# Optimization experiments

Hardware: AMD Instinct MI355X
Metric: run time of the kernel (lower is better)

## Reference

```python
import jax, jax.numpy as jnp
import numpy as np

N_NODES = 50000
N_EDGES = 800000
DIM = 64
BN_EPS = 1e-5


def setup_inputs() -> dict:
    key = jax.random.key(0)
    ks = jax.random.split(key, 9)
    s = 1.0 / np.sqrt(DIM)
    feature = jax.random.normal(ks[0], (N_NODES, DIM), jnp.float32)
    edge_index = jax.random.randint(ks[1], (2, N_EDGES), 0, N_NODES)
    Wk = jax.random.normal(ks[2], (DIM, DIM), jnp.float32) * s
    Wq = jax.random.normal(ks[3], (DIM, DIM), jnp.float32) * s
    Wv = jax.random.normal(ks[4], (DIM, DIM), jnp.float32) * s
    bk = jax.random.normal(ks[5], (DIM,), jnp.float32) * 0.01
    bq = jax.random.normal(ks[6], (DIM,), jnp.float32) * 0.01
    bv = jax.random.normal(ks[7], (DIM,), jnp.float32) * 0.01
    bias = jax.random.normal(ks[8], (DIM,), jnp.float32) * 0.01
    gamma = jnp.ones((DIM,), jnp.float32)
    beta = jnp.zeros((DIM,), jnp.float32)
    return dict(feature=feature, edge_index=edge_index, Wk=Wk, bk=bk,
                Wq=Wq, bq=bq, Wv=Wv, bv=bv, bias=bias, gamma=gamma, beta=beta)


def reference(feature, edge_index, Wk, bk, Wq, bq, Wv, bv, bias, gamma, beta):
    # Node-level projections (dense GEMMs on [N, D])
    K = feature @ Wk + bk   # applied to x_i (dst)
    Q = feature @ Wq + bq   # applied to x_j (src)
    V = feature @ Wv + bv   # applied to x_j (src)
    src, dst = edge_index[0], edge_index[1]
    # Per-edge gather -> sigmoid gate -> gated message  [E, D]
    eta = jax.nn.sigmoid(K[dst] + Q[src])
    msg = eta * V[src]
    # Scatter-add into destination nodes  [N, D]
    agg = jax.ops.segment_sum(msg, dst, num_segments=feature.shape[0])
    h = agg + bias
    # BatchNorm1d over nodes (batch statistics, biased variance) + ReLU
    mean = jnp.mean(h, axis=0)
    var = jnp.var(h, axis=0)
    h = (h - mean) * jax.lax.rsqrt(var + BN_EPS) * gamma + beta
    return jax.nn.relu(h)
```

## Files before the change

kernel.cpp:

```cpp
#include <hip/hip_runtime.h>
#include <hip/hip_fp16.h>
#include <stdint.h>

#define N_NODES 50000
#define N_EDGES 800000
#define DIM 64
#define BN_EPS 1e-5f
#define CAP 64
#define ZERO_NODE N_NODES

#define PROJ_TILES 782
#define PROJ_BLOCKS (PROJ_TILES * 3)
#define SCAT_BLOCKS 391
#define FUSED_BLOCKS (PROJ_BLOCKS + SCAT_BLOCKS)

__global__ __launch_bounds__(256) void proj_scatter_kernel(
    const float* __restrict__ feat,
    const float* __restrict__ Wk, const float* __restrict__ bk,
    const float* __restrict__ Wq, const float* __restrict__ bq,
    const float* __restrict__ Wv, const float* __restrict__ bv,
    float* __restrict__ K, __half* __restrict__ Qh, __half* __restrict__ Vh,
    const int* __restrict__ ei, int* __restrict__ counts,
    uint16_t* __restrict__ bucket)
{
  __shared__ float sW[DIM][DIM];
  __shared__ float sf[64][DIM + 4];
  __shared__ float sb[DIM];

  const int b = blockIdx.x;
  const int tid = threadIdx.x;

  if (b % 7 == 6) {
    const int sblk = b / 7;
    const int base = sblk * 2048 + tid * 8;
    if (base >= N_EDGES) return;
    if (base + 8 <= N_EDGES) {
      const int4 s0 = *(const int4*)(ei + base);
      const int4 s1 = *(const int4*)(ei + base + 4);
      const int4 d0 = *(const int4*)(ei + N_EDGES + base);
      const int4 d1 = *(const int4*)(ei + N_EDGES + base + 4);
      const int ss[8] = {s0.x, s0.y, s0.z, s0.w, s1.x, s1.y, s1.z, s1.w};
      const int dd[8] = {d0.x, d0.y, d0.z, d0.w, d1.x, d1.y, d1.z, d1.w};
      int pos[8];
#pragma unroll
      for (int i = 0; i < 8; ++i) pos[i] = atomicAdd(&counts[dd[i]], 1);
#pragma unroll
      for (int i = 0; i < 8; ++i)
        if (pos[i] < CAP) bucket[(size_t)dd[i] * CAP + pos[i]] = (uint16_t)ss[i];
    } else {
      for (int e = base; e < N_EDGES; ++e) {
        const int src = ei[e];
        const int dst = ei[N_EDGES + e];
        const int pos = atomicAdd(&counts[dst], 1);
        if (pos < CAP) bucket[(size_t)dst * CAP + pos] = (uint16_t)src;
      }
    }
    return;
  }

  const int pidx = b - b / 7;
  const int mat = pidx % 3;
  const int tile = pidx / 3;
  const float* __restrict__ W = (mat == 0) ? Wk : (mat == 1) ? Wq : Wv;
  const float* __restrict__ bb = (mat == 0) ? bk : (mat == 1) ? bq : bv;

  {
    const float4* w4 = (const float4*)W;
    float4* s4 = (float4*)&sW[0][0];
    for (int i = tid; i < DIM * DIM / 4; i += 256) s4[i] = w4[i];
  }
  if (tid < DIM) sb[tid] = bb[tid];

  const int node0 = tile * 64;
  for (int i = tid; i < 64 * 16; i += 256) {
    const int n = i >> 4, d4 = i & 15;
    const int gn = node0 + n;
    float4 v = make_float4(0.f, 0.f, 0.f, 0.f);
    if (gn < N_NODES) v = ((const float4*)feat)[gn * 16 + d4];
    *(float4*)&sf[n][d4 * 4] = v;
  }
  __syncthreads();

  const int t = tid & 15;
  const int g = tid >> 4;

  float4 a[4];
  const float4 bias = *(const float4*)&sb[t * 4];
#pragma unroll
  for (int m = 0; m < 4; ++m) a[m] = bias;

  const float4* sW4 = (const float4*)&sW[0][0];
  for (int d4 = 0; d4 < 16; ++d4) {
    const float4 w0 = sW4[(4 * d4 + 0) * 16 + t];
    const float4 w1 = sW4[(4 * d4 + 1) * 16 + t];
    const float4 w2 = sW4[(4 * d4 + 2) * 16 + t];
    const float4 w3 = sW4[(4 * d4 + 3) * 16 + t];
#pragma unroll
    for (int m = 0; m < 4; ++m) {
      const float4 f = *(const float4*)&sf[g + 16 * m][4 * d4];
      a[m].x += f.x * w0.x + f.y * w1.x + f.z * w2.x + f.w * w3.x;
      a[m].y += f.x * w0.y + f.y * w1.y + f.z * w2.y + f.w * w3.y;
      a[m].z += f.x * w0.z + f.y * w1.z + f.z * w2.z + f.w * w3.z;
      a[m].w += f.x * w0.w + f.y * w1.w + f.z * w2.w + f.w * w3.w;
    }
  }

  if (mat == 0) {
#pragma unroll
    for (int m = 0; m < 4; ++m) {
      const int gn = node0 + g + 16 * m;
      if (gn < N_NODES) ((float4*)K)[gn * 16 + t] = a[m];
    }
  } else {
    __half* __restrict__ out = (mat == 1) ? Qh : Vh;
#pragma unroll
    for (int m = 0; m < 4; ++m) {
      const int gn = node0 + g + 16 * m;
      if (gn <= N_NODES) {
        union { __half2 h[2]; uint2 u; } pk;
        pk.h[0] = __floats2half2_rn(a[m].x, a[m].y);
        pk.h[1] = __floats2half2_rn(a[m].z, a[m].w);
        if (gn == N_NODES) { pk.u.x = 0u; pk.u.y = 0u; }
        ((uint2*)out)[gn * 16 + t] = pk.u;
      }
    }
  }
}

__device__ __forceinline__ float4 edge_acc(float4 acc, const float4 k,
                                           const uint2 qu, const uint2 vu)
{
  union { uint2 u; __half2 h[2]; } q, v;
  q.u = qu; v.u = vu;
  const float2 q0 = __half22float2(q.h[0]);
  const float2 q1 = __half22float2(q.h[1]);
  const float2 v0 = __half22float2(v.h[0]);
  const float2 v1 = __half22float2(v.h[1]);
  acc.x += v0.x * __builtin_amdgcn_rcpf(1.0f + __expf(-(k.x + q0.x)));
  acc.y += v0.y * __builtin_amdgcn_rcpf(1.0f + __expf(-(k.y + q0.y)));
  acc.z += v1.x * __builtin_amdgcn_rcpf(1.0f + __expf(-(k.z + q1.x)));
  acc.w += v1.y * __builtin_amdgcn_rcpf(1.0f + __expf(-(k.w + q1.y)));
  return acc;
}

__global__ __launch_bounds__(256) void aggregate_kernel(
    const int* __restrict__ counts, const uint16_t* __restrict__ bucket,
    const float4* __restrict__ K4, const uint2* __restrict__ Qh,
    const uint2* __restrict__ Vh, float4* __restrict__ agg4)
{
  const int tid = threadIdx.x;
  const int row = tid >> 4;
  const int n = blockIdx.x * 16 + row;
  const int t = tid & 15;

  const float4 k = K4[n * 16 + t];
  int deg = counts[n];
  if (deg > CAP) deg = CAP;
  const uint16_t* bp = bucket + (size_t)n * CAP;
  float4 acc = make_float4(0.f, 0.f, 0.f, 0.f);

  for (int j0 = 0; j0 < deg; j0 += 16) {
    const int navail = deg - j0;
    const int s = (t < navail) ? (int)bp[j0 + t] : ZERO_NODE;

    int sA[8]; uint2 qA[8], vA[8];
#pragma unroll
    for (int i = 0; i < 8; ++i) sA[i] = __shfl(s, i, 16);
#pragma unroll
    for (int i = 0; i < 8; ++i) { qA[i] = Qh[sA[i] * 16 + t]; vA[i] = Vh[sA[i] * 16 + t]; }

    const bool haveB = navail > 8;
    int sB[8]; uint2 qB[8], vB[8];
    if (haveB) {
#pragma unroll
      for (int i = 0; i < 8; ++i) sB[i] = __shfl(s, 8 + i, 16);
#pragma unroll
      for (int i = 0; i < 8; ++i) { qB[i] = Qh[sB[i] * 16 + t]; vB[i] = Vh[sB[i] * 16 + t]; }
    }

#pragma unroll
    for (int i = 0; i < 8; ++i) acc = edge_acc(acc, k, qA[i], vA[i]);
    if (haveB) {
#pragma unroll
      for (int i = 0; i < 8; ++i) acc = edge_acc(acc, k, qB[i], vB[i]);
    }
  }
  agg4[n * 16 + t] = acc;
}

__global__ __launch_bounds__(256) void stats_kernel(
    const float* __restrict__ agg, float* __restrict__ stats)
{
  const int c = threadIdx.x & 63;
  const int r = threadIdx.x >> 6;
  float s = 0.0f, ss = 0.0f;
  for (int n = blockIdx.x * 4 + r; n < N_NODES; n += gridDim.x * 4) {
    const float v = agg[n * DIM + c];
    s += v; ss += v * v;
  }
  __shared__ float red[2][4][DIM];
  red[0][r][c] = s; red[1][r][c] = ss;
  __syncthreads();
  if (threadIdx.x < DIM) {
    s  = red[0][0][c] + red[0][1][c] + red[0][2][c] + red[0][3][c];
    ss = red[1][0][c] + red[1][1][c] + red[1][2][c] + red[1][3][c];
    atomicAdd(&stats[c], s);
    atomicAdd(&stats[DIM + c], ss);
  }
}

__global__ __launch_bounds__(256) void out_kernel(
    float* __restrict__ out, const float* __restrict__ stats,
    const float* __restrict__ gamma, const float* __restrict__ beta)
{
  const int idx = blockIdx.x * 256 + threadIdx.x;
  if (idx >= N_NODES * (DIM / 4)) return;
  const int t = idx & 15;
  const float4 v = ((const float4*)out)[idx];
  const float invN = 1.0f / (float)N_NODES;
  const float vin[4] = { v.x, v.y, v.z, v.w };
  float o[4];
#pragma unroll
  for (int j = 0; j < 4; ++j) {
    const int c = t * 4 + j;
    const float mean = stats[c] * invN;
    float var = stats[DIM + c] * invN - mean * mean;
    var = var < 0.0f ? 0.0f : var;
    const float scale = rsqrtf(var + BN_EPS) * gamma[c];
    const float shift = beta[c] - mean * scale;
    const float x = vin[j] * scale + shift;
    o[j] = x > 0.0f ? x : 0.0f;
  }
  float4 r; r.x = o[0]; r.y = o[1]; r.z = o[2]; r.w = o[3];
  ((float4*)out)[idx] = r;
}

extern "C" void kernel_launch(void* const* d_in, const int* in_sizes, int n_in,
                              void* d_out, int out_size, void* d_ws, size_t ws_size,
                              hipStream_t stream) {
  (void)in_sizes; (void)n_in; (void)out_size; (void)ws_size;
  const float* feat  = (const float*)d_in[0];
  const int*   ei    = (const int*)d_in[1];
  const float* Wk    = (const float*)d_in[2];
  const float* bk    = (const float*)d_in[3];
  const float* Wq    = (const float*)d_in[4];
  const float* bq    = (const float*)d_in[5];
  const float* Wv    = (const float*)d_in[6];
  const float* bv    = (const float*)d_in[7];
  const float* gamma = (const float*)d_in[9];
  const float* beta  = (const float*)d_in[10];

  char* base = (char*)d_ws;
  float*    K      = (float*)base;
  __half*   Qh     = (__half*)(base + 12800000);
  __half*   Vh     = (__half*)(base + 19200128);
  float*    stats  = (float*)(base + 25600256);
  int*      counts = (int*)(base + 25600768);
  uint16_t* bucket = (uint16_t*)(base + 25800768);

  hipMemsetAsync(stats, 0, (size_t)200512, stream);

  proj_scatter_kernel<<<FUSED_BLOCKS, 256, 0, stream>>>(
      feat, Wk, bk, Wq, bq, Wv, bv, K, Qh, Vh, ei, counts, bucket);

  aggregate_kernel<<<N_NODES / 16, 256, 0, stream>>>(
      counts, bucket, (const float4*)K, (const uint2*)Qh, (const uint2*)Vh,
      (float4*)d_out);

  stats_kernel<<<256, 256, 0, stream>>>((const float*)d_out, stats);

  out_kernel<<<(N_NODES * (DIM / 4) + 255) / 256, 256, 0, stream>>>(
      (float*)d_out, stats, gamma, beta);
}
```

Measured before the change: 184.2 us.

## Interleave Q/V rows, pad atomic counters, use 8 lanes per node in aggregate

Q and V half-precision projections are stored interleaved per node so one source row is a contiguous 256-byte gather, fetched with 16-byte loads by 8 lanes per node instead of 16 lanes with 8-byte loads. Per-node edge counters are padded to a 64-byte stride to avoid atomic contention on shared cache lines. In exchange, the memset grows from about 0.2 MB to 3.2 MB and the aggregate kernel uses more registers per lane.

```diff
diff --git a/kernel.cpp b/kernel.cpp
--- a/kernel.cpp
+++ b/kernel.cpp
@@ -8,6 +8,7 @@
 #define BN_EPS 1e-5f
 #define CAP 64
 #define ZERO_NODE N_NODES
+#define CSTRIDE 16
 
 #define PROJ_TILES 782
 #define PROJ_BLOCKS (PROJ_TILES * 3)
@@ -19,7 +20,7 @@
     const float* __restrict__ Wk, const float* __restrict__ bk,
     const float* __restrict__ Wq, const float* __restrict__ bq,
     const float* __restrict__ Wv, const float* __restrict__ bv,
-    float* __restrict__ K, __half* __restrict__ Qh, __half* __restrict__ Vh,
+    float* __restrict__ K, __half* __restrict__ QV,
     const int* __restrict__ ei, int* __restrict__ counts,
     uint16_t* __restrict__ bucket)
 {
@@ -43,7 +44,7 @@
       const int dd[8] = {d0.x, d0.y, d0.z, d0.w, d1.x, d1.y, d1.z, d1.w};
       int pos[8];
 #pragma unroll
-      for (int i = 0; i < 8; ++i) pos[i] = atomicAdd(&counts[dd[i]], 1);
+      for (int i = 0; i < 8; ++i) pos[i] = atomicAdd(&counts[dd[i] * CSTRIDE], 1);
 #pragma unroll
       for (int i = 0; i < 8; ++i)
         if (pos[i] < CAP) bucket[(size_t)dd[i] * CAP + pos[i]] = (uint16_t)ss[i];
@@ -51,7 +52,7 @@
       for (int e = base; e < N_EDGES; ++e) {
         const int src = ei[e];
         const int dst = ei[N_EDGES + e];
-        const int pos = atomicAdd(&counts[dst], 1);
+        const int pos = atomicAdd(&counts[dst * CSTRIDE], 1);
         if (pos < CAP) bucket[(size_t)dst * CAP + pos] = (uint16_t)src;
       }
     }
@@ -112,7 +113,7 @@
       if (gn < N_NODES) ((float4*)K)[gn * 16 + t] = a[m];
     }
   } else {
-    __half* __restrict__ out = (mat == 1) ? Qh : Vh;
+    const int part = (mat == 1) ? 0 : 16;
 #pragma unroll
     for (int m = 0; m < 4; ++m) {
       const int gn = node0 + g + 16 * m;
@@ -121,71 +122,72 @@
         pk.h[0] = __floats2half2_rn(a[m].x, a[m].y);
         pk.h[1] = __floats2half2_rn(a[m].z, a[m].w);
         if (gn == N_NODES) { pk.u.x = 0u; pk.u.y = 0u; }
-        ((uint2*)out)[gn * 16 + t] = pk.u;
+        ((uint2*)QV)[gn * 32 + part + t] = pk.u;
       }
     }
   }
 }
 
-__device__ __forceinline__ float4 edge_acc(float4 acc, const float4 k,
-                                           const uint2 qu, const uint2 vu)
-{
-  union { uint2 u; __half2 h[2]; } q, v;
+__device__ __forceinline__ void edge_acc8(float4& a0, float4& a1,
+                                          const float4 k0, const float4 k1,
+                                          const uint4 qu, const uint4 vu)
+{
+  union { uint4 u; __half2 h[4]; } q, v;
   q.u = qu; v.u = vu;
   const float2 q0 = __half22float2(q.h[0]);
   const float2 q1 = __half22float2(q.h[1]);
+  const float2 q2 = __half22float2(q.h[2]);
+  const float2 q3 = __half22float2(q.h[3]);
   const float2 v0 = __half22float2(v.h[0]);
   const float2 v1 = __half22float2(v.h[1]);
-  acc.x += v0.x * __builtin_amdgcn_rcpf(1.0f + __expf(-(k.x + q0.x)));
-  acc.y += v0.y * __builtin_amdgcn_rcpf(1.0f + __expf(-(k.y + q0.y)));
-  acc.z += v1.x * __builtin_amdgcn_rcpf(1.0f + __expf(-(k.z + q1.x)));
-  acc.w += v1.y * __builtin_amdgcn_rcpf(1.0f + __expf(-(k.w + q1.y)));
-  return acc;
+  const float2 v2 = __half22float2(v.h[2]);
+  const float2 v3 = __half22float2(v.h[3]);
+  a0.x += v0.x * __builtin_amdgcn_rcpf(1.0f + __expf(-(k0.x + q0.x)));
+  a0.y += v0.y * __builtin_amdgcn_rcpf(1.0f + __expf(-(k0.y + q0.y)));
+  a0.z += v1.x * __builtin_amdgcn_rcpf(1.0f + __expf(-(k0.z + q1.x)));
+  a0.w += v1.y * __builtin_amdgcn_rcpf(1.0f + __expf(-(k0.w + q1.y)));
+  a1.x += v2.x * __builtin_amdgcn_rcpf(1.0f + __expf(-(k1.x + q2.x)));
+  a1.y += v2.y * __builtin_amdgcn_rcpf(1.0f + __expf(-(k1.y + q2.y)));
+  a1.z += v3.x * __builtin_amdgcn_rcpf(1.0f + __expf(-(k1.z + q3.x)));
+  a1.w += v3.y * __builtin_amdgcn_rcpf(1.0f + __expf(-(k1.w + q3.y)));
 }
 
 __global__ __launch_bounds__(256) void aggregate_kernel(
     const int* __restrict__ counts, const uint16_t* __restrict__ bucket,
-    const float4* __restrict__ K4, const uint2* __restrict__ Qh,
-    const uint2* __restrict__ Vh, float4* __restrict__ agg4)
+    const float4* __restrict__ K4, const uint4* __restrict__ QV,
+    float4* __restrict__ agg4)
 {
   const int tid = threadIdx.x;
-  const int row = tid >> 4;
-  const int n = blockIdx.x * 16 + row;
-  const int t = tid & 15;
-
-  const float4 k = K4[n * 16 + t];
-  int deg = counts[n];
+  const int row = tid >> 3;
+  const int n = blockIdx.x * 32 + row;
+  const int t = tid & 7;
+  if (n >= N_NODES) return;
+
+  const float4 k0 = K4[n * 16 + 2 * t];
+  const float4 k1 = K4[n * 16 + 2 * t + 1];
+  int deg = counts[n * CSTRIDE];
   if (deg > CAP) deg = CAP;
   const uint16_t* bp = bucket + (size_t)n * CAP;
-  float4 acc = make_float4(0.f, 0.f, 0.f, 0.f);
-
-  for (int j0 = 0; j0 < deg; j0 += 16) {
+  float4 a0 = make_float4(0.f, 0.f, 0.f, 0.f);
+  float4 a1 = make_float4(0.f, 0.f, 0.f, 0.f);
+
+  for (int j0 = 0; j0 < deg; j0 += 8) {
     const int navail = deg - j0;
     const int s = (t < navail) ? (int)bp[j0 + t] : ZERO_NODE;
 
-    int sA[8]; uint2 qA[8], vA[8];
-#pragma unroll
-    for (int i = 0; i < 8; ++i) sA[i] = __shfl(s, i, 16);
-#pragma unroll
-    for (int i = 0; i < 8; ++i) { qA[i] = Qh[sA[i] * 16 + t]; vA[i] = Vh[sA[i] * 16 + t]; }
-
-    const bool haveB = navail > 8;
-    int sB[8]; uint2 qB[8], vB[8];
-    if (haveB) {
-#pragma unroll
-      for (int i = 0; i < 8; ++i) sB[i] = __shfl(s, 8 + i, 16);
-#pragma unroll
-      for (int i = 0; i < 8; ++i) { qB[i] = Qh[sB[i] * 16 + t]; vB[i] = Vh[sB[i] * 16 + t]; }
-    }
-
-#pragma unroll
-    for (int i = 0; i < 8; ++i) acc = edge_acc(acc, k, qA[i], vA[i]);
-    if (haveB) {
-#pragma unroll
-      for (int i = 0; i < 8; ++i) acc = edge_acc(acc, k, qB[i], vB[i]);
-    }
-  }
-  agg4[n * 16 + t] = acc;
+    int sA[8]; uint4 qA[8], vA[8];
+#pragma unroll
+    for (int i = 0; i < 8; ++i) sA[i] = __shfl(s, i, 8);
+#pragma unroll
+    for (int i = 0; i < 8; ++i) {
+      qA[i] = QV[sA[i] * 16 + t];
+      vA[i] = QV[sA[i] * 16 + 8 + t];
+    }
+#pragma unroll
+    for (int i = 0; i < 8; ++i) edge_acc8(a0, a1, k0, k1, qA[i], vA[i]);
+  }
+  agg4[n * 16 + 2 * t] = a0;
+  agg4[n * 16 + 2 * t + 1] = a1;
 }
 
 __global__ __launch_bounds__(256) void stats_kernel(
@@ -252,20 +254,18 @@
 
   char* base = (char*)d_ws;
   float*    K      = (float*)base;
-  __half*   Qh     = (__half*)(base + 12800000);
-  __half*   Vh     = (__half*)(base + 19200128);
+  __half*   QV     = (__half*)(base + 12800000);
   float*    stats  = (float*)(base + 25600256);
   int*      counts = (int*)(base + 25600768);
-  uint16_t* bucket = (uint16_t*)(base + 25800768);
-
-  hipMemsetAsync(stats, 0, (size_t)200512, stream);
+  uint16_t* bucket = (uint16_t*)(base + 28800768);
+
+  hipMemsetAsync(stats, 0, (size_t)(512 + 50000 * CSTRIDE * 4), stream);
 
   proj_scatter_kernel<<<FUSED_BLOCKS, 256, 0, stream>>>(
-      feat, Wk, bk, Wq, bq, Wv, bv, K, Qh, Vh, ei, counts, bucket);
-
-  aggregate_kernel<<<N_NODES / 16, 256, 0, stream>>>(
-      counts, bucket, (const float4*)K, (const uint2*)Qh, (const uint2*)Vh,
-      (float4*)d_out);
+      feat, Wk, bk, Wq, bq, Wv, bv, K, QV, ei, counts, bucket);
+
+  aggregate_kernel<<<(N_NODES + 31) / 32, 256, 0, stream>>>(
+      counts, bucket, (const float4*)K, (const uint4*)QV, (float4*)d_out);
 
   stats_kernel<<<256, 256, 0, stream>>>((const float*)d_out, stats);
 
```

Result: slower. 193.7 us (+5.2%).

## Fuse all stages into one persistent kernel with grid barriers

Applied to the files above, without the earlier changes.

Replaces the memset plus four kernel launches with a single persistent kernel sized to occupancy. It uses software grid barriers between phases: zeroing counts, projection and scatter, aggregation, and normalisation. Batch-norm statistics are accumulated during aggregation, which removes the separate stats pass over the output. Q and V are interleaved into one buffer so each gathered source row is contiguous. The aim is to cut launch gaps and an extra full read of the aggregate, at the cost of barrier spin overhead and lower parallelism from the persistent grid.

```diff
diff --git a/kernel.cpp b/kernel.cpp
--- a/kernel.cpp
+++ b/kernel.cpp
@@ -9,122 +9,19 @@
 #define CAP 64
 #define ZERO_NODE N_NODES
 
-#define PROJ_TILES 782
-#define PROJ_BLOCKS (PROJ_TILES * 3)
-#define SCAT_BLOCKS 391
-#define FUSED_BLOCKS (PROJ_BLOCKS + SCAT_BLOCKS)
-
-__global__ __launch_bounds__(256) void proj_scatter_kernel(
-    const float* __restrict__ feat,
-    const float* __restrict__ Wk, const float* __restrict__ bk,
-    const float* __restrict__ Wq, const float* __restrict__ bq,
-    const float* __restrict__ Wv, const float* __restrict__ bv,
-    float* __restrict__ K, __half* __restrict__ Qh, __half* __restrict__ Vh,
-    const int* __restrict__ ei, int* __restrict__ counts,
-    uint16_t* __restrict__ bucket)
-{
-  __shared__ float sW[DIM][DIM];
-  __shared__ float sf[64][DIM + 4];
-  __shared__ float sb[DIM];
-
-  const int b = blockIdx.x;
-  const int tid = threadIdx.x;
-
-  if (b % 7 == 6) {
-    const int sblk = b / 7;
-    const int base = sblk * 2048 + tid * 8;
-    if (base >= N_EDGES) return;
-    if (base + 8 <= N_EDGES) {
-      const int4 s0 = *(const int4*)(ei + base);
-      const int4 s1 = *(const int4*)(ei + base + 4);
-      const int4 d0 = *(const int4*)(ei + N_EDGES + base);
-      const int4 d1 = *(const int4*)(ei + N_EDGES + base + 4);
-      const int ss[8] = {s0.x, s0.y, s0.z, s0.w, s1.x, s1.y, s1.z, s1.w};
-      const int dd[8] = {d0.x, d0.y, d0.z, d0.w, d1.x, d1.y, d1.z, d1.w};
-      int pos[8];
-#pragma unroll
-      for (int i = 0; i < 8; ++i) pos[i] = atomicAdd(&counts[dd[i]], 1);
-#pragma unroll
-      for (int i = 0; i < 8; ++i)
-        if (pos[i] < CAP) bucket[(size_t)dd[i] * CAP + pos[i]] = (uint16_t)ss[i];
-    } else {
-      for (int e = base; e < N_EDGES; ++e) {
-        const int src = ei[e];
-        const int dst = ei[N_EDGES + e];
-        const int pos = atomicAdd(&counts[dst], 1);
-        if (pos < CAP) bucket[(size_t)dst * CAP + pos] = (uint16_t)src;
-      }
-    }
-    return;
-  }
-
-  const int pidx = b - b / 7;
-  const int mat = pidx % 3;
-  const int tile = pidx / 3;
-  const float* __restrict__ W = (mat == 0) ? Wk : (mat == 1) ? Wq : Wv;
-  const float* __restrict__ bb = (mat == 0) ? bk : (mat == 1) ? bq : bv;
-
-  {
-    const float4* w4 = (const float4*)W;
-    float4* s4 = (float4*)&sW[0][0];
-    for (int i = tid; i < DIM * DIM / 4; i += 256) s4[i] = w4[i];
-  }
-  if (tid < DIM) sb[tid] = bb[tid];
-
-  const int node0 = tile * 64;
-  for (int i = tid; i < 64 * 16; i += 256) {
-    const int n = i >> 4, d4 = i & 15;
-    const int gn = node0 + n;
-    float4 v = make_float4(0.f, 0.f, 0.f, 0.f);
-    if (gn < N_NODES) v = ((const float4*)feat)[gn * 16 + d4];
-    *(float4*)&sf[n][d4 * 4] = v;
-  }
+#define NUNITS 2737
+#define NTILES 3125
+
+__device__ __forceinline__ void grid_barrier(int* bar, int target) {
   __syncthreads();
-
-  const int t = tid & 15;
-  const int g = tid >> 4;
-
-  float4 a[4];
-  const float4 bias = *(const float4*)&sb[t * 4];
-#pragma unroll
-  for (int m = 0; m < 4; ++m) a[m] = bias;
-
-  const float4* sW4 = (const float4*)&sW[0][0];
-  for (int d4 = 0; d4 < 16; ++d4) {
-    const float4 w0 = sW4[(4 * d4 + 0) * 16 + t];
-    const float4 w1 = sW4[(4 * d4 + 1) * 16 + t];
-    const float4 w2 = sW4[(4 * d4 + 2) * 16 + t];
-    const float4 w3 = sW4[(4 * d4 + 3) * 16 + t];
-#pragma unroll
-    for (int m = 0; m < 4; ++m) {
-      const float4 f = *(const float4*)&sf[g + 16 * m][4 * d4];
-      a[m].x += f.x * w0.x + f.y * w1.x + f.z * w2.x + f.w * w3.x;
-      a[m].y += f.x * w0.y + f.y * w1.y + f.z * w2.y + f.w * w3.y;
-      a[m].z += f.x * w0.z + f.y * w1.z + f.z * w2.z + f.w * w3.z;
-      a[m].w += f.x * w0.w + f.y * w1.w + f.z * w2.w + f.w * w3.w;
-    }
-  }
-
-  if (mat == 0) {
-#pragma unroll
-    for (int m = 0; m < 4; ++m) {
-      const int gn = node0 + g + 16 * m;
-      if (gn < N_NODES) ((float4*)K)[gn * 16 + t] = a[m];
-    }
-  } else {
-    __half* __restrict__ out = (mat == 1) ? Qh : Vh;
-#pragma unroll
-    for (int m = 0; m < 4; ++m) {
-      const int gn = node0 + g + 16 * m;
-      if (gn <= N_NODES) {
-        union { __half2 h[2]; uint2 u; } pk;
-        pk.h[0] = __floats2half2_rn(a[m].x, a[m].y);
-        pk.h[1] = __floats2half2_rn(a[m].z, a[m].w);
-        if (gn == N_NODES) { pk.u.x = 0u; pk.u.y = 0u; }
-        ((uint2*)out)[gn * 16 + t] = pk.u;
-      }
-    }
-  }
+  if (threadIdx.x == 0) {
+    __threadfence_system();
+    __hip_atomic_fetch_add(bar, 1, __ATOMIC_RELAXED, __HIP_MEMORY_SCOPE_AGENT);
+    while (__hip_atomic_load(bar, __ATOMIC_RELAXED, __HIP_MEMORY_SCOPE_AGENT) < target)
+      __builtin_amdgcn_s_sleep(2);
+    __threadfence_system();
+  }
+  __syncthreads();
 }
 
 __device__ __forceinline__ float4 edge_acc(float4 acc, const float4 k,
@@ -143,96 +40,211 @@
   return acc;
 }
 
-__global__ __launch_bounds__(256) void aggregate_kernel(
-    const int* __restrict__ counts, const uint16_t* __restrict__ bucket,
-    const float4* __restrict__ K4, const uint2* __restrict__ Qh,
-    const uint2* __restrict__ Vh, float4* __restrict__ agg4)
+__global__ __launch_bounds__(256, 4) void fused_kernel(
+    const float* __restrict__ feat, const float* __restrict__ Wk,
+    const float* __restrict__ bk, const float* __restrict__ Wq,
+    const float* __restrict__ bq, const float* __restrict__ Wv,
+    const float* __restrict__ bv, const int* __restrict__ ei,
+    const float* __restrict__ gamma, const float* __restrict__ beta,
+    float* __restrict__ K, __half* __restrict__ QV,
+    int* __restrict__ counts, uint16_t* __restrict__ bucket,
+    float* __restrict__ stats, int* __restrict__ bar,
+    float* __restrict__ out)
 {
+  __shared__ __attribute__((aligned(16))) char smem[34048];
   const int tid = threadIdx.x;
-  const int row = tid >> 4;
-  const int n = blockIdx.x * 16 + row;
-  const int t = tid & 15;
-
-  const float4 k = K4[n * 16 + t];
-  int deg = counts[n];
-  if (deg > CAP) deg = CAP;
-  const uint16_t* bp = bucket + (size_t)n * CAP;
-  float4 acc = make_float4(0.f, 0.f, 0.f, 0.f);
-
-  for (int j0 = 0; j0 < deg; j0 += 16) {
-    const int navail = deg - j0;
-    const int s = (t < navail) ? (int)bp[j0 + t] : ZERO_NODE;
-
-    int sA[8]; uint2 qA[8], vA[8];
-#pragma unroll
-    for (int i = 0; i < 8; ++i) sA[i] = __shfl(s, i, 16);
-#pragma unroll
-    for (int i = 0; i < 8; ++i) { qA[i] = Qh[sA[i] * 16 + t]; vA[i] = Vh[sA[i] * 16 + t]; }
-
-    const bool haveB = navail > 8;
-    int sB[8]; uint2 qB[8], vB[8];
-    if (haveB) {
-#pragma unroll
-      for (int i = 0; i < 8; ++i) sB[i] = __shfl(s, 8 + i, 16);
-#pragma unroll
-      for (int i = 0; i < 8; ++i) { qB[i] = Qh[sB[i] * 16 + t]; vB[i] = Vh[sB[i] * 16 + t]; }
-    }
-
-#pragma unroll
-    for (int i = 0; i < 8; ++i) acc = edge_acc(acc, k, qA[i], vA[i]);
-    if (haveB) {
-#pragma unroll
-      for (int i = 0; i < 8; ++i) acc = edge_acc(acc, k, qB[i], vB[i]);
-    }
-  }
-  agg4[n * 16 + t] = acc;
-}
-
-__global__ __launch_bounds__(256) void stats_kernel(
-    const float* __restrict__ agg, float* __restrict__ stats)
-{
-  const int c = threadIdx.x & 63;
-  const int r = threadIdx.x >> 6;
-  float s = 0.0f, ss = 0.0f;
-  for (int n = blockIdx.x * 4 + r; n < N_NODES; n += gridDim.x * 4) {
-    const float v = agg[n * DIM + c];
-    s += v; ss += v * v;
-  }
-  __shared__ float red[2][4][DIM];
-  red[0][r][c] = s; red[1][r][c] = ss;
-  __syncthreads();
-  if (threadIdx.x < DIM) {
-    s  = red[0][0][c] + red[0][1][c] + red[0][2][c] + red[0][3][c];
-    ss = red[1][0][c] + red[1][1][c] + red[1][2][c] + red[1][3][c];
-    atomicAdd(&stats[c], s);
-    atomicAdd(&stats[DIM + c], ss);
-  }
-}
-
-__global__ __launch_bounds__(256) void out_kernel(
-    float* __restrict__ out, const float* __restrict__ stats,
-    const float* __restrict__ gamma, const float* __restrict__ beta)
-{
-  const int idx = blockIdx.x * 256 + threadIdx.x;
-  if (idx >= N_NODES * (DIM / 4)) return;
-  const int t = idx & 15;
-  const float4 v = ((const float4*)out)[idx];
-  const float invN = 1.0f / (float)N_NODES;
-  const float vin[4] = { v.x, v.y, v.z, v.w };
-  float o[4];
-#pragma unroll
-  for (int j = 0; j < 4; ++j) {
-    const int c = t * 4 + j;
-    const float mean = stats[c] * invN;
-    float var = stats[DIM + c] * invN - mean * mean;
-    var = var < 0.0f ? 0.0f : var;
-    const float scale = rsqrtf(var + BN_EPS) * gamma[c];
-    const float shift = beta[c] - mean * scale;
-    const float x = vin[j] * scale + shift;
-    o[j] = x > 0.0f ? x : 0.0f;
-  }
-  float4 r; r.x = o[0]; r.y = o[1]; r.z = o[2]; r.w = o[3];
-  ((float4*)out)[idx] = r;
+  const int bid = blockIdx.x;
+  const int nblk = gridDim.x;
+  const int nthr = nblk * 256;
+
+  for (int i = bid * 256 + tid; i < N_NODES; i += nthr) counts[i] = 0;
+  if (bid == 0 && tid < 128) stats[tid] = 0.0f;
+  grid_barrier(bar, nblk);
+
+  {
+    float* sW = (float*)smem;
+    float* sf = (float*)(smem + 16384);
+    float* sb = (float*)(smem + 33792);
+
+    for (int u = bid; u < NUNITS; u += nblk) {
+      if (u % 7 == 6) {
+        const int base = (u / 7) * 2048 + tid * 8;
+        if (base + 8 <= N_EDGES) {
+          const int4 s0 = *(const int4*)(ei + base);
+          const int4 s1 = *(const int4*)(ei + base + 4);
+          const int4 d0 = *(const int4*)(ei + N_EDGES + base);
+          const int4 d1 = *(const int4*)(ei + N_EDGES + base + 4);
+          const int ss[8] = {s0.x, s0.y, s0.z, s0.w, s1.x, s1.y, s1.z, s1.w};
+          const int dd[8] = {d0.x, d0.y, d0.z, d0.w, d1.x, d1.y, d1.z, d1.w};
+          int pos[8];
+#pragma unroll
+          for (int i = 0; i < 8; ++i) pos[i] = atomicAdd(&counts[dd[i]], 1);
+#pragma unroll
+          for (int i = 0; i < 8; ++i)
+            if (pos[i] < CAP) bucket[(size_t)dd[i] * CAP + pos[i]] = (uint16_t)ss[i];
+        }
+      } else {
+        const int pidx = u - u / 7;
+        const int mat = pidx % 3;
+        const int tile = pidx / 3;
+        const float* __restrict__ W = (mat == 0) ? Wk : (mat == 1) ? Wq : Wv;
+        const float* __restrict__ bb = (mat == 0) ? bk : (mat == 1) ? bq : bv;
+
+        __syncthreads();
+        {
+          const float4* w4 = (const float4*)W;
+          float4* s4 = (float4*)sW;
+          for (int i = tid; i < DIM * DIM / 4; i += 256) s4[i] = w4[i];
+        }
+        if (tid < DIM) sb[tid] = bb[tid];
+        const int node0 = tile * 64;
+        for (int i = tid; i < 64 * 16; i += 256) {
+          const int n = i >> 4, d4 = i & 15;
+          const int gn = node0 + n;
+          float4 v = make_float4(0.f, 0.f, 0.f, 0.f);
+          if (gn < N_NODES) v = ((const float4*)feat)[gn * 16 + d4];
+          *(float4*)&sf[n * 68 + d4 * 4] = v;
+        }
+        __syncthreads();
+
+        const int t = tid & 15;
+        const int g = tid >> 4;
+        float4 a[4];
+        const float4 bias = *(const float4*)&sb[t * 4];
+#pragma unroll
+        for (int m = 0; m < 4; ++m) a[m] = bias;
+
+        const float4* sW4 = (const float4*)sW;
+        for (int d4 = 0; d4 < 16; ++d4) {
+          const float4 w0 = sW4[(4 * d4 + 0) * 16 + t];
+          const float4 w1 = sW4[(4 * d4 + 1) * 16 + t];
+          const float4 w2 = sW4[(4 * d4 + 2) * 16 + t];
+          const float4 w3 = sW4[(4 * d4 + 3) * 16 + t];
+#pragma unroll
+          for (int m = 0; m < 4; ++m) {
+            const float4 f = *(const float4*)&sf[(g + 16 * m) * 68 + 4 * d4];
+            a[m].x += f.x * w0.x + f.y * w1.x + f.z * w2.x + f.w * w3.x;
+            a[m].y += f.x * w0.y + f.y * w1.y + f.z * w2.y + f.w * w3.y;
+            a[m].z += f.x * w0.z + f.y * w1.z + f.z * w2.z + f.w * w3.z;
+            a[m].w += f.x * w0.w + f.y * w1.w + f.z * w2.w + f.w * w3.w;
+          }
+        }
+
+        if (mat == 0) {
+#pragma unroll
+          for (int m = 0; m < 4; ++m) {
+            const int gn = node0 + g + 16 * m;
+            if (gn < N_NODES) ((float4*)K)[gn * 16 + t] = a[m];
+          }
+        } else {
+          const int part = (mat == 1) ? 0 : 16;
+#pragma unroll
+          for (int m = 0; m < 4; ++m) {
+            const int gn = node0 + g + 16 * m;
+            if (gn <= N_NODES) {
+              union { __half2 h[2]; uint2 u2; } pk;
+              pk.h[0] = __floats2half2_rn(a[m].x, a[m].y);
+              pk.h[1] = __floats2half2_rn(a[m].z, a[m].w);
+              if (gn == N_NODES) { pk.u2.x = 0u; pk.u2.y = 0u; }
+              ((uint2*)QV)[gn * 32 + part + t] = pk.u2;
+            }
+          }
+        }
+      }
+    }
+  }
+  grid_barrier(bar, 2 * nblk);
+
+  {
+    const int row = tid >> 4;
+    const int t = tid & 15;
+    const uint2* QV2 = (const uint2*)QV;
+    float4 psum = make_float4(0.f, 0.f, 0.f, 0.f);
+    float4 pssq = make_float4(0.f, 0.f, 0.f, 0.f);
+
+    for (int tile = bid; tile < NTILES; tile += nblk) {
+      const int n = tile * 16 + row;
+      const float4 k = ((const float4*)K)[n * 16 + t];
+      int deg = counts[n];
+      if (deg > CAP) deg = CAP;
+      const uint16_t* bp = bucket + (size_t)n * CAP;
+      float4 acc = make_float4(0.f, 0.f, 0.f, 0.f);
+
+      for (int j0 = 0; j0 < deg; j0 += 16) {
+        const int navail = deg - j0;
+        const int s = (t < navail) ? (int)bp[j0 + t] : ZERO_NODE;
+
+        int sA[8]; uint2 qA[8], vA[8];
+#pragma unroll
+        for (int i = 0; i < 8; ++i) sA[i] = __shfl(s, i, 16);
+#pragma unroll
+        for (int i = 0; i < 8; ++i) {
+          qA[i] = QV2[sA[i] * 32 + t];
+          vA[i] = QV2[sA[i] * 32 + 16 + t];
+        }
+        const bool haveB = navail > 8;
+        int sB[8]; uint2 qB[8], vB[8];
+        if (haveB) {
+#pragma unroll
+          for (int i = 0; i < 8; ++i) sB[i] = __shfl(s, 8 + i, 16);
+#pragma unroll
+          for (int i = 0; i < 8; ++i) {
+            qB[i] = QV2[sB[i] * 32 + t];
+            vB[i] = QV2[sB[i] * 32 + 16 + t];
+          }
+        }
+#pragma unroll
+        for (int i = 0; i < 8; ++i) acc = edge_acc(acc, k, qA[i], vA[i]);
+        if (haveB) {
+#pragma unroll
+          for (int i = 0; i < 8; ++i) acc = edge_acc(acc, k, qB[i], vB[i]);
+        }
+      }
+      ((float4*)out)[n * 16 + t] = acc;
+      psum.x += acc.x; psum.y += acc.y; psum.z += acc.z; psum.w += acc.w;
+      pssq.x += acc.x * acc.x; pssq.y += acc.y * acc.y;
+      pssq.z += acc.z * acc.z; pssq.w += acc.w * acc.w;
+    }
+
+    __syncthreads();
+    float* sred = (float*)smem;
+    *(float4*)&sred[row * 68 + t * 4] = psum;
+    *(float4*)&sred[(16 + row) * 68 + t * 4] = pssq;
+    __syncthreads();
+    if (tid < 128) {
+      const int s = tid >> 6, c = tid & 63;
+      float v = 0.0f;
+#pragma unroll
+      for (int r = 0; r < 16; ++r) v += sred[(s * 16 + r) * 68 + c];
+      atomicAdd(&stats[tid], v);
+    }
+  }
+  grid_barrier(bar, 3 * nblk);
+
+  {
+    const int i0 = bid * 256 + tid;
+    const int t = i0 & 15;
+    const float invN = 1.0f / (float)N_NODES;
+    float scale[4], shift[4];
+#pragma unroll
+    for (int j = 0; j < 4; ++j) {
+      const int c = t * 4 + j;
+      const float mean = stats[c] * invN;
+      float var = stats[DIM + c] * invN - mean * mean;
+      var = var < 0.0f ? 0.0f : var;
+      scale[j] = rsqrtf(var + BN_EPS) * gamma[c];
+      shift[j] = beta[c] - mean * scale[j];
+    }
+    for (int idx = i0; idx < N_NODES * 16; idx += nthr) {
+      const float4 v = ((const float4*)out)[idx];
+      float4 r;
+      r.x = v.x * scale[0] + shift[0]; r.x = r.x > 0.f ? r.x : 0.f;
+      r.y = v.y * scale[1] + shift[1]; r.y = r.y > 0.f ? r.y : 0.f;
+      r.z = v.z * scale[2] + shift[2]; r.z = r.z > 0.f ? r.z : 0.f;
+      r.w = v.w * scale[3] + shift[3]; r.w = r.w > 0.f ? r.w : 0.f;
+      ((float4*)out)[idx] = r;
+    }
+  }
 }
 
 extern "C" void kernel_launch(void* const* d_in, const int* in_sizes, int n_in,
@@ -252,23 +264,22 @@
 
   char* base = (char*)d_ws;
   float*    K      = (float*)base;
-  __half*   Qh     = (__half*)(base + 12800000);
-  __half*   Vh     = (__half*)(base + 19200128);
+  __half*   QV     = (__half*)(base + 12800000);
   float*    stats  = (float*)(base + 25600256);
-  int*      counts = (int*)(base + 25600768);
-  uint16_t* bucket = (uint16_t*)(base + 25800768);
-
-  hipMemsetAsync(stats, 0, (size_t)200512, stream);
-
-  proj_scatter_kernel<<<FUSED_BLOCKS, 256, 0, stream>>>(
-      feat, Wk, bk, Wq, bq, Wv, bv, K, Qh, Vh, ei, counts, bucket);
-
-  aggregate_kernel<<<N_NODES / 16, 256, 0, stream>>>(
-      counts, bucket, (const float4*)K, (const uint2*)Qh, (const uint2*)Vh,
-      (float4*)d_out);
-
-  stats_kernel<<<256, 256, 0, stream>>>((const float*)d_out, stats);
-
-  out_kernel<<<(N_NODES * (DIM / 4) + 255) / 256, 256, 0, stream>>>(
-      (float*)d_out, stats, gamma, beta);
-}
+  int*      bar    = (int*)(base + 25600768);
+  int*      counts = (int*)(base + 25600832);
+  uint16_t* bucket = (uint16_t*)(base + 25800832);
+
+  (void)hipMemsetAsync(bar, 0, 64, stream);
+
+  int mb = 0;
+  if (hipOccupancyMaxActiveBlocksPerMultiprocessor(&mb, fused_kernel, 256, 0)
+          != hipSuccess || mb < 1)
+    mb = 1;
+  int nblk = mb * 256;
+  if (nblk > 1024) nblk = 1024;
+
+  fused_kernel<<<nblk, 256, 0, stream>>>(
+      feat, Wk, bk, Wq, bq, Wv, bv, ei, gamma, beta,
+      K, QV, counts, bucket, stats, bar, (float*)d_out);
+}
```

Result: slower. 486.8 us (+164.3%).
